# Optimization experiments

Hardware: AMD Instinct MI355X
Metric: run time of the kernel (lower is better)

The kernel has to match this reference:

```python
import jax, jax.numpy as jnp
import numpy as np

B, DIM, Hs, Ws = 2, 64, 48, 48
HEADS, DIM_HEAD = 4, 16
INNER = HEADS * DIM_HEAD  # 64
MLP_DIM = 256


def setup_inputs() -> dict:
    key = jax.random.key(0)
    ks = jax.random.split(key, 10)
    w = lambda k, shape: (jax.random.normal(k, shape, jnp.float32) * 0.02)
    return dict(
        x=jax.random.normal(ks[0], (B, DIM, Hs, Ws), jnp.float32),
        y=jax.random.normal(ks[1], (B, DIM, Hs, Ws), jnp.float32),
        ln1_g=jnp.ones((DIM,), jnp.float32), ln1_b=jnp.zeros((DIM,), jnp.float32),
        w_sa1=w(ks[2], (DIM, INNER)), w_sa2=w(ks[3], (DIM, INNER)),
        w_se1=w(ks[4], (DIM, INNER)), w_se2=w(ks[5], (DIM, INNER)),
        w_out=w(ks[6], (INNER, DIM)), b_out=jnp.zeros((DIM,), jnp.float32),
        ln2_g=jnp.ones((DIM,), jnp.float32), ln2_b=jnp.zeros((DIM,), jnp.float32),
        w1=w(ks[7], (DIM, MLP_DIM)), b1=jnp.zeros((MLP_DIM,), jnp.float32),
        w2=w(ks[8], (MLP_DIM, DIM)), b2=jnp.zeros((DIM,), jnp.float32),
    )


def _layer_norm(t, g, b, eps=1e-5):
    m = t.mean(-1, keepdims=True)
    v = t.var(-1, keepdims=True)
    return (t - m) * jax.lax.rsqrt(v + eps) * g + b


def reference(x, y, ln1_g, ln1_b, w_sa1, w_sa2, w_se1, w_se2, w_out, b_out,
              ln2_g, ln2_b, w1, b1, w2, b2):
    b, c, h, wdt = x.shape
    xt = x.reshape(b, c, h * wdt).transpose(0, 2, 1)  # B n C
    yt = y.reshape(b, c, h * wdt).transpose(0, 2, 1)
    n = xt.shape[1]
    scale = DIM_HEAD ** (-0.5)

    # PreNorm: same LayerNorm applied to both x and y (shared params)
    xn = _layer_norm(xt, ln1_g, ln1_b)
    yn = _layer_norm(yt, ln1_g, ln1_b)

    def split_heads(t, wm):  # B n C -> B h n d
        return (t @ wm).reshape(b, n, HEADS, DIM_HEAD).transpose(0, 2, 1, 3)

    y1 = split_heads(yn, w_sa1)
    y2 = split_heads(yn, w_sa2)
    x1 = split_heads(xn, w_se1)
    x2 = split_heads(xn, w_se2)

    # spatial attention map: n x n from y branch
    sacm = jax.nn.softmax(jnp.einsum('bhid,bhjd->bhij', y1, y2) * scale, axis=-1)
    # channel attention map: d x d from x branch
    secm = jax.nn.softmax(jnp.einsum('bhni,bhnj->bhij', x1, x2) * scale / (n / DIM_HEAD), axis=-1)

    out1 = jnp.einsum('bhij,bhjd->bhid', sacm, x1)  # spatial map applied to x values
    out2 = jnp.einsum('bhni,bhij->bhnj', y1, secm)  # channel map applied to y values
    out = (out1 * out2).transpose(0, 2, 1, 3).reshape(b, n, INNER)
    xt = xt + out @ w_out + b_out  # residual around attention

    # MLP with PreNorm + residual, LeakyReLU slope 0.01 (torch default)
    xn2 = _layer_norm(xt, ln2_g, ln2_b)
    hid = jax.nn.leaky_relu(xn2 @ w1 + b1, negative_slope=0.01)
    xt = xt + hid @ w2 + b2

    return xt.transpose(0, 2, 1).reshape(b, c, h, wdt)
```

## Files before the change

kernel.cpp:

```cpp
#include <hip/hip_runtime.h>

#define HW 2304
#define CH 64
typedef unsigned short ushort_t;
typedef __attribute__((ext_vector_type(8))) short bf16x8;
typedef __attribute__((ext_vector_type(4))) float f32x4;

#define QSCL (0.25f * 1.44269504088896340736f)
#define SECM_SCL (0.25f / 144.f)
#define MFMA(a, b, c) __builtin_amdgcn_mfma_f32_16x16x32_bf16((a), (b), (c), 0, 0, 0)

static __device__ __forceinline__ ushort_t f2bf(float f) {
    union { float f; unsigned u; } v; v.f = f;
    unsigned r = v.u + 0x7FFFu + ((v.u >> 16) & 1u);
    return (ushort_t)(r >> 16);
}
static __device__ __forceinline__ unsigned cvtpk(float a, float b) {
    unsigned r;
    asm("v_cvt_pk_bf16_f32 %0, %1, %2" : "=v"(r) : "v"(a), "v"(b));
    return r;
}
union U8 { unsigned u[4]; bf16x8 v; };

__global__ __launch_bounds__(256) void k_wconv(
    const float* __restrict__ wsa1, const float* __restrict__ wsa2,
    const float* __restrict__ wse1, const float* __restrict__ wse2,
    const float* __restrict__ w_out, const float* __restrict__ w1,
    const float* __restrict__ w2,
    ushort_t* __restrict__ wsa1T, ushort_t* __restrict__ wsa2T,
    ushort_t* __restrict__ wse1T, ushort_t* __restrict__ wse2T,
    ushort_t* __restrict__ w_outT, ushort_t* __restrict__ wT1, ushort_t* __restrict__ wT2,
    float* __restrict__ sacc)
{
    const int blk = blockIdx.x, tid = threadIdx.x;
    if (blk < 8) sacc[blk * 256 + tid] = 0.f;
    if (blk < 80) {
        const int mi = blk >> 4;
        const float* s = mi == 0 ? wsa1 : mi == 1 ? wsa2 : mi == 2 ? wse1 : mi == 3 ? wse2 : w_out;
        ushort_t* d = mi == 0 ? wsa1T : mi == 1 ? wsa2T : mi == 2 ? wse1T : mi == 3 ? wse2T : w_outT;
        const int o = (blk & 15) * 256 + tid;
        d[o] = f2bf(s[(o & 63) * 64 + (o >> 6)]);
    } else if (blk < 144) {
        const int o = (blk - 80) * 256 + tid;
        wT1[o] = f2bf(w1[(o & 63) * 256 + (o >> 6)]);
    } else {
        const int o = (blk - 144) * 256 + tid;
        wT2[o] = f2bf(w2[(o & 255) * 64 + (o >> 8)]);
    }
}

__global__ __launch_bounds__(64) void k_ln_proj(
    const float* __restrict__ x, const float* __restrict__ y,
    const float* __restrict__ g, const float* __restrict__ bb,
    const ushort_t* __restrict__ wsa1T, const ushort_t* __restrict__ wsa2T,
    const ushort_t* __restrict__ wse1T, const ushort_t* __restrict__ wse2T,
    float* __restrict__ y1f, ushort_t* __restrict__ qbf, ushort_t* __restrict__ kbf,
    ushort_t* __restrict__ vtbf, float* __restrict__ sacc)
{
    __shared__ ushort_t ldsA[16 * 24 + 32];
    __shared__ ushort_t ldsB[16 * 24 + 32];
    const int task = blockIdx.x;
    const int rt = task % 144;
    const int b  = (task / 144) & 1;
    const int branch = task / 288;
    const int lane = threadIdx.x;
    const int r = lane & 15, cg = lane >> 4;
    const int q0 = rt * 16;
    const float* in = (branch ? y : x) + (size_t)b * CH * HW + q0 + r;
    float lo[8], hi[8];
    float s = 0.f, sq = 0.f;
    #pragma unroll
    for (int ki = 0; ki < 8; ++ki) {
        lo[ki] = in[(size_t)(8 * cg + ki) * HW];
        hi[ki] = in[(size_t)(32 + 8 * cg + ki) * HW];
        s += lo[ki] + hi[ki];
        sq += lo[ki] * lo[ki] + hi[ki] * hi[ki];
    }
    s  += __shfl_xor(s, 16);  s  += __shfl_xor(s, 32);
    sq += __shfl_xor(sq, 16); sq += __shfl_xor(sq, 32);
    const float m  = s * (1.f / 64.f);
    const float rs = rsqrtf(sq * (1.f / 64.f) - m * m + 1e-5f);
    float ga[16], be[16];
    {
        const float4* gp = (const float4*)g;
        const float4* bp = (const float4*)bb;
        *(float4*)&ga[0]  = gp[2 * cg];     *(float4*)&ga[4]  = gp[2 * cg + 1];
        *(float4*)&ga[8]  = gp[8 + 2 * cg]; *(float4*)&ga[12] = gp[9 + 2 * cg];
        *(float4*)&be[0]  = bp[2 * cg];     *(float4*)&be[4]  = bp[2 * cg + 1];
        *(float4*)&be[8]  = bp[8 + 2 * cg]; *(float4*)&be[12] = bp[9 + 2 * cg];
    }
    float nlo[8], nhi[8];
    #pragma unroll
    for (int ki = 0; ki < 8; ++ki) {
        nlo[ki] = (lo[ki] - m) * rs * ga[ki]     + be[ki];
        nhi[ki] = (hi[ki] - m) * rs * ga[8 + ki] + be[8 + ki];
    }
    U8 alo, ahi;
    #pragma unroll
    for (int p = 0; p < 4; ++p) {
        alo.u[p] = cvtpk(nlo[2 * p], nlo[2 * p + 1]);
        ahi.u[p] = cvtpk(nhi[2 * p], nhi[2 * p + 1]);
    }
    const ushort_t* wp1 = branch ? wsa1T : wse1T;
    const ushort_t* wp2 = branch ? wsa2T : wse2T;
    const f32x4 zero4 = {0.f, 0.f, 0.f, 0.f};
    #pragma unroll
    for (int jt = 0; jt < 4; ++jt) {
        const int bh = b * 4 + jt;
        bf16x8 bl1 = *(const bf16x8*)(wp1 + (jt * 16 + r) * 64 + 8 * cg);
        bf16x8 bh1 = *(const bf16x8*)(wp1 + (jt * 16 + r) * 64 + 32 + 8 * cg);
        f32x4 acc1 = zero4;
        acc1 = MFMA(alo.v, bl1, acc1);
        acc1 = MFMA(ahi.v, bh1, acc1);
        bf16x8 bl2 = *(const bf16x8*)(wp2 + (jt * 16 + r) * 64 + 8 * cg);
        bf16x8 bh2 = *(const bf16x8*)(wp2 + (jt * 16 + r) * 64 + 32 + 8 * cg);
        f32x4 acc2 = zero4;
        acc2 = MFMA(alo.v, bl2, acc2);
        acc2 = MFMA(ahi.v, bh2, acc2);
        if (branch == 0) {
            uint2 pk1; pk1.x = cvtpk(acc1[0], acc1[1]); pk1.y = cvtpk(acc1[2], acc1[3]);
            *(uint2*)(vtbf + (size_t)(bh * 16 + r) * HW + q0 + 4 * cg) = pk1;
            *(uint2*)&ldsA[r * 24 + 4 * cg] = pk1;
            uint2 pk2; pk2.x = cvtpk(acc2[0], acc2[1]); pk2.y = cvtpk(acc2[2], acc2[3]);
            *(uint2*)&ldsB[r * 24 + 4 * cg] = pk2;
            bf16x8 af = {0, 0, 0, 0, 0, 0, 0, 0};
            bf16x8 bf_ = {0, 0, 0, 0, 0, 0, 0, 0};
            if (cg < 2) {
                af  = *(const bf16x8*)&ldsA[r * 24 + 8 * cg];
                bf_ = *(const bf16x8*)&ldsB[r * 24 + 8 * cg];
            }
            f32x4 sp = MFMA(af, bf_, zero4);
            #pragma unroll
            for (int ri = 0; ri < 4; ++ri)
                atomicAdd(&sacc[bh * 256 + (4 * cg + ri) * 16 + r], sp[ri]);
        } else {
            #pragma unroll
            for (int ri = 0; ri < 4; ++ri) {
                const int q = q0 + 4 * cg + ri;
                y1f[((size_t)bh * HW + q) * 16 + r] = acc1[ri];
                qbf[((size_t)bh * HW + q) * 16 + r] = f2bf(acc1[ri] * QSCL);
                kbf[((size_t)bh * HW + q) * 16 + r] = f2bf(acc2[ri]);
            }
        }
    }
}

__global__ __launch_bounds__(256, 4) void k_attn(
    const ushort_t* __restrict__ qbf, const ushort_t* __restrict__ kbf,
    const ushort_t* __restrict__ vtbf, const float* __restrict__ y1f,
    const float* __restrict__ sacc, ushort_t* __restrict__ obf)
{
    __shared__ uint4 pbuf4[4][80];
    __shared__ f32x4 cacc[4][64];
    __shared__ float clsum[4][64];
    __shared__ float sraw[256];
    __shared__ float smv[256];
    const int qt = blockIdx.x, bh = blockIdx.y;
    const int tid = threadIdx.x;
    const int w = tid >> 6, lane = tid & 63;
    const int q16 = lane & 15, g = lane >> 4;
    const int q0 = qt * 16;
    const float v = sacc[bh * 256 + tid] * SECM_SCL;
    sraw[tid] = v;
    __syncthreads();
    {
        const int i = tid >> 4;
        float mx = -1e30f;
        #pragma unroll
        for (int jj = 0; jj < 16; ++jj) mx = fmaxf(mx, sraw[i * 16 + jj]);
        float sum = 0.f;
        #pragma unroll
        for (int jj = 0; jj < 16; ++jj) sum += __expf(sraw[i * 16 + jj] - mx);
        smv[tid] = __expf(v - mx) / sum;
    }

    bf16x8 qfrag = {0, 0, 0, 0, 0, 0, 0, 0};
    if (g < 2) qfrag = *(const bf16x8*)(qbf + ((size_t)bh * HW + q0 + q16) * 16 + g * 8);

    unsigned char* pw = (unsigned char*)&pbuf4[w][0];
    const ushort_t* kbase = kbf + (size_t)bh * HW * 16;
    const ushort_t* vbase = vtbf + (size_t)(bh * 16 + q16) * HW;
    f32x4 oacc = {0.f, 0.f, 0.f, 0.f};
    float lsum = 0.f;
    const f32x4 zero4 = {0.f, 0.f, 0.f, 0.f};

    #pragma unroll 2
    for (int wi = 0; wi < 18; ++wi) {
        const int k0 = w * 576 + wi * 32;
        bf16x8 kf0 = *(const bf16x8*)(kbase + (size_t)(k0 + q16) * 16 + (g & 1) * 8);
        bf16x8 kf1 = *(const bf16x8*)(kbase + (size_t)(k0 + 16 + q16) * 16 + (g & 1) * 8);
        f32x4 s0 = MFMA(kf0, qfrag, zero4);
        f32x4 s1 = MFMA(kf1, qfrag, zero4);
        const float e00 = exp2f(s0[0]), e01 = exp2f(s0[1]), e02 = exp2f(s0[2]), e03 = exp2f(s0[3]);
        const float e10 = exp2f(s1[0]), e11 = exp2f(s1[1]), e12 = exp2f(s1[2]), e13 = exp2f(s1[3]);
        lsum += ((e00 + e01) + (e02 + e03)) + ((e10 + e11) + (e12 + e13));
        *(unsigned*)(pw + q16 * 80 + 8 * g)      = cvtpk(e00, e01);
        *(unsigned*)(pw + q16 * 80 + 8 * g + 4)  = cvtpk(e02, e03);
        *(unsigned*)(pw + q16 * 80 + 32 + 8 * g) = cvtpk(e10, e11);
        *(unsigned*)(pw + q16 * 80 + 36 + 8 * g) = cvtpk(e12, e13);
        bf16x8 vfrag = *(const bf16x8*)(vbase + k0 + 8 * g);
        bf16x8 pfrag = *(const bf16x8*)(pw + q16 * 80 + 16 * g);
        oacc = MFMA(vfrag, pfrag, oacc);
    }
    cacc[w][lane] = oacc;
    clsum[w][lane] = lsum;
    __syncthreads();
    if (tid < 64) {
        f32x4 t0 = cacc[0][lane], t1 = cacc[1][lane], t2 = cacc[2][lane], t3 = cacc[3][lane];
        float L = clsum[0][lane] + clsum[1][lane] + clsum[2][lane] + clsum[3][lane];
        L += __shfl_xor(L, 16);
        L += __shfl_xor(L, 32);
        const float invl = 1.f / L;
        const float* yrow = y1f + ((size_t)bh * HW + q0 + q16) * 16;
        float ya[16];
        #pragma unroll
        for (int i = 0; i < 4; ++i) *(float4*)&ya[4 * i] = ((const float4*)yrow)[i];
        float gate[4] = {0.f, 0.f, 0.f, 0.f};
        #pragma unroll
        for (int i = 0; i < 16; ++i) {
            #pragma unroll
            for (int rr = 0; rr < 4; ++rr) gate[rr] += ya[i] * smv[i * 16 + g * 4 + rr];
        }
        const int b = bh >> 2, h = bh & 3;
        float r0 = (t0[0] + t1[0] + t2[0] + t3[0]) * invl * gate[0];
        float r1 = (t0[1] + t1[1] + t2[1] + t3[1]) * invl * gate[1];
        float r2 = (t0[2] + t1[2] + t2[2] + t3[2]) * invl * gate[2];
        float r3 = (t0[3] + t1[3] + t2[3] + t3[3]) * invl * gate[3];
        uint2 pk; pk.x = cvtpk(r0, r1); pk.y = cvtpk(r2, r3);
        *(uint2*)(obf + ((size_t)b * HW + q0 + q16) * 64 + h * 16 + g * 4) = pk;
    }
}

__global__ __launch_bounds__(64) void k_tail(
    const ushort_t* __restrict__ obf, const float* __restrict__ x,
    const ushort_t* __restrict__ w_outT, const float* __restrict__ b_out,
    const float* __restrict__ g2, const float* __restrict__ bt2,
    const ushort_t* __restrict__ wT1, const float* __restrict__ b1,
    const ushort_t* __restrict__ wT2, const float* __restrict__ b2,
    float* __restrict__ out)
{
    __shared__ ushort_t xn[16 * 72 + 16];
    __shared__ ushort_t hh[16 * 264 + 16];
    const int t = blockIdx.x;
    const int b = t / 144;
    const int q0 = (t % 144) * 16;
    const int lane = threadIdx.x, r = lane & 15, cg = lane >> 4;
    const f32x4 zero4 = {0.f, 0.f, 0.f, 0.f};
    const ushort_t* arow = obf + ((size_t)b * HW + q0 + r) * 64;
    bf16x8 alo = *(const bf16x8*)(arow + 8 * cg);
    bf16x8 ahi = *(const bf16x8*)(arow + 32 + 8 * cg);
    float xt[4][4];
    #pragma unroll
    for (int jt = 0; jt < 4; ++jt) {
        bf16x8 bl = *(const bf16x8*)(w_outT + (jt * 16 + r) * 64 + 8 * cg);
        bf16x8 bh_ = *(const bf16x8*)(w_outT + (jt * 16 + r) * 64 + 32 + 8 * cg);
        f32x4 acc = zero4;
        acc = MFMA(alo, bl, acc);
        acc = MFMA(ahi, bh_, acc);
        const int c = jt * 16 + r;
        const float bo = b_out[c];
        float4 xr = *(const float4*)(x + (size_t)b * CH * HW + (size_t)c * HW + q0 + 4 * cg);
        xt[jt][0] = acc[0] + bo + xr.x;
        xt[jt][1] = acc[1] + bo + xr.y;
        xt[jt][2] = acc[2] + bo + xr.z;
        xt[jt][3] = acc[3] + bo + xr.w;
    }
    float mr[4], rv[4];
    #pragma unroll
    for (int ri = 0; ri < 4; ++ri) {
        float s  = xt[0][ri] + xt[1][ri] + xt[2][ri] + xt[3][ri];
        float sq = xt[0][ri] * xt[0][ri] + xt[1][ri] * xt[1][ri]
                 + xt[2][ri] * xt[2][ri] + xt[3][ri] * xt[3][ri];
        s  += __shfl_xor(s, 1);  s  += __shfl_xor(s, 2);
        s  += __shfl_xor(s, 4);  s  += __shfl_xor(s, 8);
        sq += __shfl_xor(sq, 1); sq += __shfl_xor(sq, 2);
        sq += __shfl_xor(sq, 4); sq += __shfl_xor(sq, 8);
        mr[ri] = s * (1.f / 64.f);
        rv[ri] = rsqrtf(sq * (1.f / 64.f) - mr[ri] * mr[ri] + 1e-5f);
    }
    #pragma unroll
    for (int jt = 0; jt < 4; ++jt) {
        const int c = jt * 16 + r;
        const float gg = g2[c], bb = bt2[c];
        #pragma unroll
        for (int ri = 0; ri < 4; ++ri) {
            const float val = (xt[jt][ri] - mr[ri]) * rv[ri] * gg + bb;
            xn[(4 * cg + ri) * 72 + c] = f2bf(val);
        }
    }
    bf16x8 axlo = *(const bf16x8*)&xn[r * 72 + 8 * cg];
    bf16x8 axhi = *(const bf16x8*)&xn[r * 72 + 32 + 8 * cg];
    #pragma unroll 4
    for (int jt = 0; jt < 16; ++jt) {
        bf16x8 bl = *(const bf16x8*)(wT1 + (jt * 16 + r) * 64 + 8 * cg);
        bf16x8 bh_ = *(const bf16x8*)(wT1 + (jt * 16 + r) * 64 + 32 + 8 * cg);
        f32x4 acc = zero4;
        acc = MFMA(axlo, bl, acc);
        acc = MFMA(axhi, bh_, acc);
        const int c = jt * 16 + r;
        const float bias = b1[c];
        #pragma unroll
        for (int ri = 0; ri < 4; ++ri) {
            float vv = acc[ri] + bias;
            vv = fmaxf(vv, 0.01f * vv);
            hh[(4 * cg + ri) * 264 + c] = f2bf(vv);
        }
    }
    bf16x8 ha[8];
    #pragma unroll
    for (int kw = 0; kw < 8; ++kw)
        ha[kw] = *(const bf16x8*)&hh[r * 264 + kw * 32 + 8 * cg];
    #pragma unroll
    for (int jt = 0; jt < 4; ++jt) {
        f32x4 acc = zero4;
        #pragma unroll
        for (int kw = 0; kw < 8; ++kw) {
            bf16x8 bf_ = *(const bf16x8*)(wT2 + (jt * 16 + r) * 256 + kw * 32 + 8 * cg);
            acc = MFMA(ha[kw], bf_, acc);
        }
        const int c = jt * 16 + r;
        const float bias = b2[c];
        float4 res;
        res.x = acc[0] + bias + xt[jt][0];
        res.y = acc[1] + bias + xt[jt][1];
        res.z = acc[2] + bias + xt[jt][2];
        res.w = acc[3] + bias + xt[jt][3];
        *(float4*)(out + (size_t)b * CH * HW + (size_t)c * HW + q0 + 4 * cg) = res;
    }
}

extern "C" void kernel_launch(void* const* d_in, const int* in_sizes, int n_in,
                              void* d_out, int out_size, void* d_ws, size_t ws_size,
                              hipStream_t stream)
{
    (void)in_sizes; (void)n_in; (void)out_size; (void)ws_size;
    const float* x     = (const float*)d_in[0];
    const float* y     = (const float*)d_in[1];
    const float* ln1_g = (const float*)d_in[2];
    const float* ln1_b = (const float*)d_in[3];
    const float* w_sa1 = (const float*)d_in[4];
    const float* w_sa2 = (const float*)d_in[5];
    const float* w_se1 = (const float*)d_in[6];
    const float* w_se2 = (const float*)d_in[7];
    const float* w_out = (const float*)d_in[8];
    const float* b_out = (const float*)d_in[9];
    const float* ln2_g = (const float*)d_in[10];
    const float* ln2_b = (const float*)d_in[11];
    const float* w1    = (const float*)d_in[12];
    const float* b1    = (const float*)d_in[13];
    const float* w2    = (const float*)d_in[14];
    const float* b2    = (const float*)d_in[15];
    float* out = (float*)d_out;

    const size_t NP = 8ull * HW * 16;
    float* p = (float*)d_ws;
    float* y1f  = p;  p += NP;
    float* sacc = p;  p += 2048;
    ushort_t* u = (ushort_t*)p;
    ushort_t* qbf   = u;  u += NP;
    ushort_t* kbf   = u;  u += NP;
    ushort_t* vtbf  = u;  u += NP;
    ushort_t* obf   = u;  u += NP;
    ushort_t* wsa1T = u;  u += 4096;
    ushort_t* wsa2T = u;  u += 4096;
    ushort_t* wse1T = u;  u += 4096;
    ushort_t* wse2T = u;  u += 4096;
    ushort_t* w_outT= u;  u += 4096;
    ushort_t* wT1   = u;  u += 16384;
    ushort_t* wT2   = u;  u += 16384;

    k_wconv<<<208, 256, 0, stream>>>(w_sa1, w_sa2, w_se1, w_se2, w_out, w1, w2,
                                     wsa1T, wsa2T, wse1T, wse2T, w_outT, wT1, wT2,
                                     sacc);
    k_ln_proj<<<576, 64, 0, stream>>>(x, y, ln1_g, ln1_b,
                                      wsa1T, wsa2T, wse1T, wse2T,
                                      y1f, qbf, kbf, vtbf, sacc);
    k_attn<<<dim3(144, 8), 256, 0, stream>>>(qbf, kbf, vtbf, y1f, sacc, obf);
    k_tail<<<288, 64, 0, stream>>>(obf, x, w_outT, b_out, ln2_g, ln2_b,
                                   wT1, b1, wT2, b2, out);
}
```

Baseline: 126.9 us.

## Spread work across more waves in projection, attention and tail kernels

The projection kernel gains a grid dimension so each block handles one head instead of looping over four. The attention kernel uses 8 waves per block, each covering half as many keys, and reduces partial results across 8 waves. The tail kernel moves from one wave to four, with the LayerNorm going through a shared float tile and each wave computing a slice of the output and MLP columns. This exposes more parallelism and latency hiding for a small problem, at the cost of recomputing LayerNorm per head in the projection, extra barriers, and a larger cross-wave reduction.

After: 119.3 us. -6.0%, faster.

```diff
diff --git a/kernel.cpp b/kernel.cpp
--- a/kernel.cpp
+++ b/kernel.cpp
@@ -60,6 +60,7 @@
     __shared__ ushort_t ldsA[16 * 24 + 32];
     __shared__ ushort_t ldsB[16 * 24 + 32];
     const int task = blockIdx.x;
+    const int jt = blockIdx.y;
     const int rt = task % 144;
     const int b  = (task / 144) & 1;
     const int branch = task / 288;
@@ -104,55 +105,52 @@
     const ushort_t* wp1 = branch ? wsa1T : wse1T;
     const ushort_t* wp2 = branch ? wsa2T : wse2T;
     const f32x4 zero4 = {0.f, 0.f, 0.f, 0.f};
-    #pragma unroll
-    for (int jt = 0; jt < 4; ++jt) {
-        const int bh = b * 4 + jt;
-        bf16x8 bl1 = *(const bf16x8*)(wp1 + (jt * 16 + r) * 64 + 8 * cg);
-        bf16x8 bh1 = *(const bf16x8*)(wp1 + (jt * 16 + r) * 64 + 32 + 8 * cg);
-        f32x4 acc1 = zero4;
-        acc1 = MFMA(alo.v, bl1, acc1);
-        acc1 = MFMA(ahi.v, bh1, acc1);
-        bf16x8 bl2 = *(const bf16x8*)(wp2 + (jt * 16 + r) * 64 + 8 * cg);
-        bf16x8 bh2 = *(const bf16x8*)(wp2 + (jt * 16 + r) * 64 + 32 + 8 * cg);
-        f32x4 acc2 = zero4;
-        acc2 = MFMA(alo.v, bl2, acc2);
-        acc2 = MFMA(ahi.v, bh2, acc2);
-        if (branch == 0) {
-            uint2 pk1; pk1.x = cvtpk(acc1[0], acc1[1]); pk1.y = cvtpk(acc1[2], acc1[3]);
-            *(uint2*)(vtbf + (size_t)(bh * 16 + r) * HW + q0 + 4 * cg) = pk1;
-            *(uint2*)&ldsA[r * 24 + 4 * cg] = pk1;
-            uint2 pk2; pk2.x = cvtpk(acc2[0], acc2[1]); pk2.y = cvtpk(acc2[2], acc2[3]);
-            *(uint2*)&ldsB[r * 24 + 4 * cg] = pk2;
-            bf16x8 af = {0, 0, 0, 0, 0, 0, 0, 0};
-            bf16x8 bf_ = {0, 0, 0, 0, 0, 0, 0, 0};
-            if (cg < 2) {
-                af  = *(const bf16x8*)&ldsA[r * 24 + 8 * cg];
-                bf_ = *(const bf16x8*)&ldsB[r * 24 + 8 * cg];
-            }
-            f32x4 sp = MFMA(af, bf_, zero4);
-            #pragma unroll
-            for (int ri = 0; ri < 4; ++ri)
-                atomicAdd(&sacc[bh * 256 + (4 * cg + ri) * 16 + r], sp[ri]);
-        } else {
-            #pragma unroll
-            for (int ri = 0; ri < 4; ++ri) {
-                const int q = q0 + 4 * cg + ri;
-                y1f[((size_t)bh * HW + q) * 16 + r] = acc1[ri];
-                qbf[((size_t)bh * HW + q) * 16 + r] = f2bf(acc1[ri] * QSCL);
-                kbf[((size_t)bh * HW + q) * 16 + r] = f2bf(acc2[ri]);
-            }
-        }
-    }
-}
-
-__global__ __launch_bounds__(256, 4) void k_attn(
+    const int bh = b * 4 + jt;
+    bf16x8 bl1 = *(const bf16x8*)(wp1 + (jt * 16 + r) * 64 + 8 * cg);
+    bf16x8 bh1 = *(const bf16x8*)(wp1 + (jt * 16 + r) * 64 + 32 + 8 * cg);
+    f32x4 acc1 = zero4;
+    acc1 = MFMA(alo.v, bl1, acc1);
+    acc1 = MFMA(ahi.v, bh1, acc1);
+    bf16x8 bl2 = *(const bf16x8*)(wp2 + (jt * 16 + r) * 64 + 8 * cg);
+    bf16x8 bh2 = *(const bf16x8*)(wp2 + (jt * 16 + r) * 64 + 32 + 8 * cg);
+    f32x4 acc2 = zero4;
+    acc2 = MFMA(alo.v, bl2, acc2);
+    acc2 = MFMA(ahi.v, bh2, acc2);
+    if (branch == 0) {
+        uint2 pk1; pk1.x = cvtpk(acc1[0], acc1[1]); pk1.y = cvtpk(acc1[2], acc1[3]);
+        *(uint2*)(vtbf + (size_t)(bh * 16 + r) * HW + q0 + 4 * cg) = pk1;
+        *(uint2*)&ldsA[r * 24 + 4 * cg] = pk1;
+        uint2 pk2; pk2.x = cvtpk(acc2[0], acc2[1]); pk2.y = cvtpk(acc2[2], acc2[3]);
+        *(uint2*)&ldsB[r * 24 + 4 * cg] = pk2;
+        bf16x8 af = {0, 0, 0, 0, 0, 0, 0, 0};
+        bf16x8 bf_ = {0, 0, 0, 0, 0, 0, 0, 0};
+        if (cg < 2) {
+            af  = *(const bf16x8*)&ldsA[r * 24 + 8 * cg];
+            bf_ = *(const bf16x8*)&ldsB[r * 24 + 8 * cg];
+        }
+        f32x4 sp = MFMA(af, bf_, zero4);
+        #pragma unroll
+        for (int ri = 0; ri < 4; ++ri)
+            atomicAdd(&sacc[bh * 256 + (4 * cg + ri) * 16 + r], sp[ri]);
+    } else {
+        #pragma unroll
+        for (int ri = 0; ri < 4; ++ri) {
+            const int q = q0 + 4 * cg + ri;
+            y1f[((size_t)bh * HW + q) * 16 + r] = acc1[ri];
+            qbf[((size_t)bh * HW + q) * 16 + r] = f2bf(acc1[ri] * QSCL);
+            kbf[((size_t)bh * HW + q) * 16 + r] = f2bf(acc2[ri]);
+        }
+    }
+}
+
+__global__ __launch_bounds__(512) void k_attn(
     const ushort_t* __restrict__ qbf, const ushort_t* __restrict__ kbf,
     const ushort_t* __restrict__ vtbf, const float* __restrict__ y1f,
     const float* __restrict__ sacc, ushort_t* __restrict__ obf)
 {
-    __shared__ uint4 pbuf4[4][80];
-    __shared__ f32x4 cacc[4][64];
-    __shared__ float clsum[4][64];
+    __shared__ uint4 pbuf4[8][80];
+    __shared__ f32x4 cacc[8][64];
+    __shared__ float clsum[8][64];
     __shared__ float sraw[256];
     __shared__ float smv[256];
     const int qt = blockIdx.x, bh = blockIdx.y;
@@ -160,10 +158,9 @@
     const int w = tid >> 6, lane = tid & 63;
     const int q16 = lane & 15, g = lane >> 4;
     const int q0 = qt * 16;
-    const float v = sacc[bh * 256 + tid] * SECM_SCL;
-    sraw[tid] = v;
+    if (tid < 256) sraw[tid] = sacc[bh * 256 + tid] * SECM_SCL;
     __syncthreads();
-    {
+    if (tid < 256) {
         const int i = tid >> 4;
         float mx = -1e30f;
         #pragma unroll
@@ -171,7 +168,7 @@
         float sum = 0.f;
         #pragma unroll
         for (int jj = 0; jj < 16; ++jj) sum += __expf(sraw[i * 16 + jj] - mx);
-        smv[tid] = __expf(v - mx) / sum;
+        smv[tid] = __expf(sraw[tid] - mx) / sum;
     }
 
     bf16x8 qfrag = {0, 0, 0, 0, 0, 0, 0, 0};
@@ -184,9 +181,9 @@
     float lsum = 0.f;
     const f32x4 zero4 = {0.f, 0.f, 0.f, 0.f};
 
-    #pragma unroll 2
-    for (int wi = 0; wi < 18; ++wi) {
-        const int k0 = w * 576 + wi * 32;
+    #pragma unroll 3
+    for (int wi = 0; wi < 9; ++wi) {
+        const int k0 = w * 288 + wi * 32;
         bf16x8 kf0 = *(const bf16x8*)(kbase + (size_t)(k0 + q16) * 16 + (g & 1) * 8);
         bf16x8 kf1 = *(const bf16x8*)(kbase + (size_t)(k0 + 16 + q16) * 16 + (g & 1) * 8);
         f32x4 s0 = MFMA(kf0, qfrag, zero4);
@@ -206,8 +203,14 @@
     clsum[w][lane] = lsum;
     __syncthreads();
     if (tid < 64) {
-        f32x4 t0 = cacc[0][lane], t1 = cacc[1][lane], t2 = cacc[2][lane], t3 = cacc[3][lane];
-        float L = clsum[0][lane] + clsum[1][lane] + clsum[2][lane] + clsum[3][lane];
+        f32x4 t = cacc[0][lane];
+        float L = clsum[0][lane];
+        #pragma unroll
+        for (int ww = 1; ww < 8; ++ww) {
+            f32x4 tw = cacc[ww][lane];
+            t[0] += tw[0]; t[1] += tw[1]; t[2] += tw[2]; t[3] += tw[3];
+            L += clsum[ww][lane];
+        }
         L += __shfl_xor(L, 16);
         L += __shfl_xor(L, 32);
         const float invl = 1.f / L;
@@ -222,16 +225,16 @@
             for (int rr = 0; rr < 4; ++rr) gate[rr] += ya[i] * smv[i * 16 + g * 4 + rr];
         }
         const int b = bh >> 2, h = bh & 3;
-        float r0 = (t0[0] + t1[0] + t2[0] + t3[0]) * invl * gate[0];
-        float r1 = (t0[1] + t1[1] + t2[1] + t3[1]) * invl * gate[1];
-        float r2 = (t0[2] + t1[2] + t2[2] + t3[2]) * invl * gate[2];
-        float r3 = (t0[3] + t1[3] + t2[3] + t3[3]) * invl * gate[3];
+        float r0 = t[0] * invl * gate[0];
+        float r1 = t[1] * invl * gate[1];
+        float r2 = t[2] * invl * gate[2];
+        float r3 = t[3] * invl * gate[3];
         uint2 pk; pk.x = cvtpk(r0, r1); pk.y = cvtpk(r2, r3);
         *(uint2*)(obf + ((size_t)b * HW + q0 + q16) * 64 + h * 16 + g * 4) = pk;
     }
 }
 
-__global__ __launch_bounds__(64) void k_tail(
+__global__ __launch_bounds__(256) void k_tail(
     const ushort_t* __restrict__ obf, const float* __restrict__ x,
     const ushort_t* __restrict__ w_outT, const float* __restrict__ b_out,
     const float* __restrict__ g2, const float* __restrict__ bt2,
@@ -239,64 +242,72 @@
     const ushort_t* __restrict__ wT2, const float* __restrict__ b2,
     float* __restrict__ out)
 {
-    __shared__ ushort_t xn[16 * 72 + 16];
+    __shared__ float xtile[16][68];
     __shared__ ushort_t hh[16 * 264 + 16];
     const int t = blockIdx.x;
     const int b = t / 144;
     const int q0 = (t % 144) * 16;
-    const int lane = threadIdx.x, r = lane & 15, cg = lane >> 4;
+    const int tid = threadIdx.x;
+    const int w = tid >> 6, lane = tid & 63;
+    const int r = lane & 15, cg = lane >> 4;
     const f32x4 zero4 = {0.f, 0.f, 0.f, 0.f};
     const ushort_t* arow = obf + ((size_t)b * HW + q0 + r) * 64;
     bf16x8 alo = *(const bf16x8*)(arow + 8 * cg);
     bf16x8 ahi = *(const bf16x8*)(arow + 32 + 8 * cg);
-    float xt[4][4];
-    #pragma unroll
-    for (int jt = 0; jt < 4; ++jt) {
-        bf16x8 bl = *(const bf16x8*)(w_outT + (jt * 16 + r) * 64 + 8 * cg);
-        bf16x8 bh_ = *(const bf16x8*)(w_outT + (jt * 16 + r) * 64 + 32 + 8 * cg);
+    {
+        bf16x8 bl = *(const bf16x8*)(w_outT + (w * 16 + r) * 64 + 8 * cg);
+        bf16x8 bh_ = *(const bf16x8*)(w_outT + (w * 16 + r) * 64 + 32 + 8 * cg);
         f32x4 acc = zero4;
         acc = MFMA(alo, bl, acc);
         acc = MFMA(ahi, bh_, acc);
-        const int c = jt * 16 + r;
+        const int c = w * 16 + r;
         const float bo = b_out[c];
         float4 xr = *(const float4*)(x + (size_t)b * CH * HW + (size_t)c * HW + q0 + 4 * cg);
-        xt[jt][0] = acc[0] + bo + xr.x;
-        xt[jt][1] = acc[1] + bo + xr.y;
-        xt[jt][2] = acc[2] + bo + xr.z;
-        xt[jt][3] = acc[3] + bo + xr.w;
-    }
-    float mr[4], rv[4];
-    #pragma unroll
-    for (int ri = 0; ri < 4; ++ri) {
-        float s  = xt[0][ri] + xt[1][ri] + xt[2][ri] + xt[3][ri];
-        float sq = xt[0][ri] * xt[0][ri] + xt[1][ri] * xt[1][ri]
-                 + xt[2][ri] * xt[2][ri] + xt[3][ri] * xt[3][ri];
-        s  += __shfl_xor(s, 1);  s  += __shfl_xor(s, 2);
-        s  += __shfl_xor(s, 4);  s  += __shfl_xor(s, 8);
-        sq += __shfl_xor(sq, 1); sq += __shfl_xor(sq, 2);
-        sq += __shfl_xor(sq, 4); sq += __shfl_xor(sq, 8);
-        mr[ri] = s * (1.f / 64.f);
-        rv[ri] = rsqrtf(sq * (1.f / 64.f) - mr[ri] * mr[ri] + 1e-5f);
-    }
-    #pragma unroll
-    for (int jt = 0; jt < 4; ++jt) {
-        const int c = jt * 16 + r;
-        const float gg = g2[c], bb = bt2[c];
-        #pragma unroll
-        for (int ri = 0; ri < 4; ++ri) {
-            const float val = (xt[jt][ri] - mr[ri]) * rv[ri] * gg + bb;
-            xn[(4 * cg + ri) * 72 + c] = f2bf(val);
-        }
-    }
-    bf16x8 axlo = *(const bf16x8*)&xn[r * 72 + 8 * cg];
-    bf16x8 axhi = *(const bf16x8*)&xn[r * 72 + 32 + 8 * cg];
-    #pragma unroll 4
-    for (int jt = 0; jt < 16; ++jt) {
+        xtile[4 * cg + 0][c] = acc[0] + bo + xr.x;
+        xtile[4 * cg + 1][c] = acc[1] + bo + xr.y;
+        xtile[4 * cg + 2][c] = acc[2] + bo + xr.z;
+        xtile[4 * cg + 3][c] = acc[3] + bo + xr.w;
+    }
+    __syncthreads();
+    float s = 0.f, sq = 0.f;
+    #pragma unroll
+    for (int j = 0; j < 16; ++j) {
+        const float v = xtile[r][cg * 16 + j];
+        s += v; sq += v * v;
+    }
+    s  += __shfl_xor(s, 16);  s  += __shfl_xor(s, 32);
+    sq += __shfl_xor(sq, 16); sq += __shfl_xor(sq, 32);
+    const float m  = s * (1.f / 64.f);
+    const float rs = rsqrtf(sq * (1.f / 64.f) - m * m + 1e-5f);
+    float ga[16], be[16];
+    {
+        const float4* gp = (const float4*)g2;
+        const float4* bp = (const float4*)bt2;
+        *(float4*)&ga[0]  = gp[2 * cg];     *(float4*)&ga[4]  = gp[2 * cg + 1];
+        *(float4*)&ga[8]  = gp[8 + 2 * cg]; *(float4*)&ga[12] = gp[9 + 2 * cg];
+        *(float4*)&be[0]  = bp[2 * cg];     *(float4*)&be[4]  = bp[2 * cg + 1];
+        *(float4*)&be[8]  = bp[8 + 2 * cg]; *(float4*)&be[12] = bp[9 + 2 * cg];
+    }
+    float nlo[8], nhi[8];
+    #pragma unroll
+    for (int ki = 0; ki < 8; ++ki) {
+        nlo[ki] = (xtile[r][8 * cg + ki]      - m) * rs * ga[ki]     + be[ki];
+        nhi[ki] = (xtile[r][32 + 8 * cg + ki] - m) * rs * ga[8 + ki] + be[8 + ki];
+    }
+    U8 axlo, axhi;
+    #pragma unroll
+    for (int p = 0; p < 4; ++p) {
+        axlo.u[p] = cvtpk(nlo[2 * p], nlo[2 * p + 1]);
+        axhi.u[p] = cvtpk(nhi[2 * p], nhi[2 * p + 1]);
+    }
+    #pragma unroll
+    for (int jj = 0; jj < 4; ++jj) {
+        const int jt = 4 * w + jj;
         bf16x8 bl = *(const bf16x8*)(wT1 + (jt * 16 + r) * 64 + 8 * cg);
         bf16x8 bh_ = *(const bf16x8*)(wT1 + (jt * 16 + r) * 64 + 32 + 8 * cg);
         f32x4 acc = zero4;
-        acc = MFMA(axlo, bl, acc);
-        acc = MFMA(axhi, bh_, acc);
+        acc = MFMA(axlo.v, bl, acc);
+        acc = MFMA(axhi.v, bh_, acc);
         const int c = jt * 16 + r;
         const float bias = b1[c];
         #pragma unroll
@@ -306,27 +317,25 @@
             hh[(4 * cg + ri) * 264 + c] = f2bf(vv);
         }
     }
+    __syncthreads();
     bf16x8 ha[8];
     #pragma unroll
     for (int kw = 0; kw < 8; ++kw)
         ha[kw] = *(const bf16x8*)&hh[r * 264 + kw * 32 + 8 * cg];
-    #pragma unroll
-    for (int jt = 0; jt < 4; ++jt) {
-        f32x4 acc = zero4;
-        #pragma unroll
-        for (int kw = 0; kw < 8; ++kw) {
-            bf16x8 bf_ = *(const bf16x8*)(wT2 + (jt * 16 + r) * 256 + kw * 32 + 8 * cg);
-            acc = MFMA(ha[kw], bf_, acc);
-        }
-        const int c = jt * 16 + r;
-        const float bias = b2[c];
-        float4 res;
-        res.x = acc[0] + bias + xt[jt][0];
-        res.y = acc[1] + bias + xt[jt][1];
-        res.z = acc[2] + bias + xt[jt][2];
-        res.w = acc[3] + bias + xt[jt][3];
-        *(float4*)(out + (size_t)b * CH * HW + (size_t)c * HW + q0 + 4 * cg) = res;
-    }
+    f32x4 acc = zero4;
+    #pragma unroll
+    for (int kw = 0; kw < 8; ++kw) {
+        bf16x8 bf_ = *(const bf16x8*)(wT2 + (w * 16 + r) * 256 + kw * 32 + 8 * cg);
+        acc = MFMA(ha[kw], bf_, acc);
+    }
+    const int c = w * 16 + r;
+    const float bias = b2[c];
+    float4 res;
+    res.x = acc[0] + bias + xtile[4 * cg + 0][c];
+    res.y = acc[1] + bias + xtile[4 * cg + 1][c];
+    res.z = acc[2] + bias + xtile[4 * cg + 2][c];
+    res.w = acc[3] + bias + xtile[4 * cg + 3][c];
+    *(float4*)(out + (size_t)b * CH * HW + (size_t)c * HW + q0 + 4 * cg) = res;
 }
 
 extern "C" void kernel_launch(void* const* d_in, const int* in_sizes, int n_in,
@@ -372,10 +381,10 @@
     k_wconv<<<208, 256, 0, stream>>>(w_sa1, w_sa2, w_se1, w_se2, w_out, w1, w2,
                                      wsa1T, wsa2T, wse1T, wse2T, w_outT, wT1, wT2,
                                      sacc);
-    k_ln_proj<<<576, 64, 0, stream>>>(x, y, ln1_g, ln1_b,
-                                      wsa1T, wsa2T, wse1T, wse2T,
-                                      y1f, qbf, kbf, vtbf, sacc);
-    k_attn<<<dim3(144, 8), 256, 0, stream>>>(qbf, kbf, vtbf, y1f, sacc, obf);
-    k_tail<<<288, 64, 0, stream>>>(obf, x, w_outT, b_out, ln2_g, ln2_b,
-                                   wT1, b1, wT2, b2, out);
-}
+    k_ln_proj<<<dim3(576, 4), 64, 0, stream>>>(x, y, ln1_g, ln1_b,
+                                               wsa1T, wsa2T, wse1T, wse2T,
+                                               y1f, qbf, kbf, vtbf, sacc);
+    k_attn<<<dim3(144, 8), 512, 0, stream>>>(qbf, kbf, vtbf, y1f, sacc, obf);
+    k_tail<<<288, 256, 0, stream>>>(obf, x, w_outT, b_out, ln2_g, ln2_b,
+                                    wT1, b1, wT2, b2, out);
+}
```
